# Optimization experiments

Measured on AMD Instinct MI355X. Metric: run time of the kernel, lower is better.

Reference implementation:

```python
import jax, jax.numpy as jnp
import numpy as np

D_MODEL = 256
N_LAYERS = 2
EXPAND = 2
D_INNER = EXPAND * D_MODEL  # 512
D_STATE = 16
D_CONV = 4
DT_RANK = max(1, D_MODEL // 16)  # 16


def _selective_scan(x, dt, B, C, A, D):
    # x, dt: [b, l, d]   B, C: [b, l, n]   A: [d, n]   D: [d]
    dA = jnp.exp(jnp.einsum('bld,dn->bldn', dt, A))          # discretized state matrix
    dBx = jnp.einsum('bld,bln,bld->bldn', dt, B, x)           # dt * B * u

    def step(h, inp):
        dA_t, dBx_t, C_t = inp                                 # [b,d,n],[b,d,n],[b,n]
        h = dA_t * h + dBx_t
        y = jnp.einsum('bdn,bn->bd', h, C_t)
        return h, y

    h0 = jnp.zeros((x.shape[0], A.shape[0], A.shape[1]), x.dtype)
    _, ys = jax.lax.scan(step, h0, (jnp.moveaxis(dA, 1, 0),
                                    jnp.moveaxis(dBx, 1, 0),
                                    jnp.moveaxis(C, 1, 0)))
    return jnp.moveaxis(ys, 0, 1) + x * D                      # [b, l, d]


def _mamba_block(z, in_w, conv_w, conv_b, xp_w, dt_w, dt_b, A_log, Dp, out_w):
    b, l, _ = z.shape
    xz = z @ in_w.T                                            # [b, l, 2*d_inner]
    x, gate = jnp.split(xz, 2, axis=-1)
    # causal depthwise conv1d over time
    xt = jnp.transpose(x, (0, 2, 1))                            # [b, d_inner, l]
    xt = jax.lax.conv_general_dilated(
        xt, conv_w[:, None, :], window_strides=(1,),
        padding=[(D_CONV - 1, 0)], feature_group_count=D_INNER)
    x = jax.nn.silu(jnp.transpose(xt, (0, 2, 1)) + conv_b)      # [b, l, d_inner]
    x_dbl = x @ xp_w.T                                          # [b, l, dt_rank + 2*d_state]
    dt, Bm, Cm = jnp.split(x_dbl, [DT_RANK, DT_RANK + D_STATE], axis=-1)
    dt = jax.nn.softplus(dt @ dt_w.T + dt_b)                    # [b, l, d_inner]
    A = -jnp.exp(A_log)                                         # [d_inner, d_state]
    y = _selective_scan(x, dt, Bm, Cm, A, Dp)
    y = y * jax.nn.silu(gate)
    return y @ out_w.T                                          # [b, l, d_model]


def setup_inputs() -> dict:
    key = jax.random.key(0)
    ks = jax.random.split(key, 9)
    B, L = 2, 4096
    z = jax.random.normal(ks[0], (B, L, D_MODEL), jnp.float32)
    s = 0.02
    in_proj_w = jax.random.normal(ks[1], (N_LAYERS, 2 * D_INNER, D_MODEL), jnp.float32) * s
    conv_w = jax.random.normal(ks[2], (N_LAYERS, D_INNER, D_CONV), jnp.float32) * 0.2
    conv_b = jnp.zeros((N_LAYERS, D_INNER), jnp.float32)
    x_proj_w = jax.random.normal(ks[3], (N_LAYERS, DT_RANK + 2 * D_STATE, D_INNER), jnp.float32) * s
    dt_proj_w = jax.random.normal(ks[4], (N_LAYERS, D_INNER, DT_RANK), jnp.float32) * 0.1
    dt_proj_b = jax.random.uniform(ks[5], (N_LAYERS, D_INNER), jnp.float32, -4.0, -2.0)
    A_log = jnp.log(jnp.broadcast_to(jnp.arange(1, D_STATE + 1, dtype=jnp.float32),
                                     (N_LAYERS, D_INNER, D_STATE)))
    D_param = jnp.ones((N_LAYERS, D_INNER), jnp.float32)
    out_proj_w = jax.random.normal(ks[6], (N_LAYERS, D_MODEL, D_INNER), jnp.float32) * s
    return {"z": z, "in_proj_w": in_proj_w, "conv_w": conv_w, "conv_b": conv_b,
            "x_proj_w": x_proj_w, "dt_proj_w": dt_proj_w, "dt_proj_b": dt_proj_b,
            "A_log": A_log, "D_param": D_param, "out_proj_w": out_proj_w}


def reference(z, in_proj_w, conv_w, conv_b, x_proj_w, dt_proj_w, dt_proj_b,
              A_log, D_param, out_proj_w):
    for i in range(N_LAYERS):
        z = _mamba_block(z, in_proj_w[i], conv_w[i], conv_b[i], x_proj_w[i],
                         dt_proj_w[i], dt_proj_b[i], A_log[i], D_param[i], out_proj_w[i])
    return z
```

## Files before the change

kernel.cpp:

```cpp
#include <hip/hip_runtime.h>
#include <hip/hip_bf16.h>
#include <cstdint>
#include <cstddef>

#define DM   256
#define DI   512
#define DS   16
#define LSEQ 4096
#define BATCH 2
#define BLROWS (BATCH * LSEQ)
#define NCH  128
#define CLEN 32
#define XCP  520

typedef __bf16 bf16x8 __attribute__((ext_vector_type(8)));
typedef float  f32x4  __attribute__((ext_vector_type(4)));
typedef unsigned short u16;
typedef u16 u16x8 __attribute__((ext_vector_type(8)));
typedef u16 u16x4 __attribute__((ext_vector_type(4)));

__device__ __forceinline__ u16 f2bfu(float f) {
    union { float f; unsigned u; } c; c.f = f;
    unsigned u = c.u;
    return (u16)((u + 0x7fffu + ((u >> 16) & 1u)) >> 16);
}
__device__ __forceinline__ float bfu2f(u16 u) {
    union { unsigned u; float f; } c; c.u = ((unsigned)u) << 16; return c.f;
}
__device__ __forceinline__ float siluf(float v) {
    return v * (1.0f / (1.0f + __expf(-v)));
}
__device__ __forceinline__ void gload_lds16(const void* g, void* l) {
    __builtin_amdgcn_global_load_lds(
        (const __attribute__((address_space(1))) unsigned int*)g,
        (__attribute__((address_space(3))) unsigned int*)l, 16, 0, 0);
}

#define N_INW  (2*1024*256)
#define N_OUTW (2*256*512)
#define N_XPW  (2*64*512)
#define N_Z    (BLROWS*DM)
__global__ __launch_bounds__(256) void cast_all_k(
    const float* __restrict__ in_w, const float* __restrict__ out_w,
    const float* __restrict__ xp_w, const float* __restrict__ z,
    u16* __restrict__ inw_bf, u16* __restrict__ outw_bf,
    u16* __restrict__ xpw_bf, u16* __restrict__ z_bf) {
    int i = blockIdx.x * 256 + threadIdx.x;
    if (i < N_INW) {
        inw_bf[i] = f2bfu(in_w[i]);
    } else if (i < N_INW + N_OUTW) {
        int j = i - N_INW;
        outw_bf[j] = f2bfu(out_w[j]);
    } else if (i < N_INW + N_OUTW + N_XPW) {
        int j = i - (N_INW + N_OUTW);
        int k = j & 511, o = (j >> 9) & 63, l = j >> 15;
        xpw_bf[j] = f2bfu((o < 48) ? xp_w[(l * 48 + o) * 512 + k] : 0.0f);
    } else {
        int j = i - (N_INW + N_OUTW + N_XPW);
        z_bf[j] = f2bfu(z[j]);
    }
}

__global__ __launch_bounds__(256) void gemm_in_k(
    const __bf16* __restrict__ A, const __bf16* __restrict__ B,
    u16* __restrict__ Cb, int M, int N, int K) {
    __shared__ __bf16 As[128 * 32];
    __shared__ __bf16 Bs[128 * 32];
    int tid = threadIdx.x, wave = tid >> 6, lane = tid & 63;
    int bm = blockIdx.x * 128, bn = blockIdx.y * 128;
    int wm = (wave & 1) * 64, wn = (wave >> 1) * 64;
    int row = lane & 15, q = lane >> 4;
    int srow = lane >> 2, sseg = lane & 3;
    f32x4 acc[4][4] = {};
    for (int k0 = 0; k0 < K; k0 += 32) {
        #pragma unroll
        for (int i = 0; i < 2; ++i) {
            int r0 = wave * 32 + i * 16;
            gload_lds16(A + (size_t)(bm + r0 + srow) * K + k0 + sseg * 8, As + r0 * 32);
            gload_lds16(B + (size_t)(bn + r0 + srow) * K + k0 + sseg * 8, Bs + r0 * 32);
        }
        __syncthreads();
        bf16x8 af[4], bfr[4];
        #pragma unroll
        for (int mi = 0; mi < 4; ++mi)
            af[mi] = *(const bf16x8*)&As[(wm + mi*16 + row) * 32 + q * 8];
        #pragma unroll
        for (int ni = 0; ni < 4; ++ni)
            bfr[ni] = *(const bf16x8*)&Bs[(wn + ni*16 + row) * 32 + q * 8];
        #pragma unroll
        for (int mi = 0; mi < 4; ++mi)
            #pragma unroll
            for (int ni = 0; ni < 4; ++ni)
                acc[mi][ni] = __builtin_amdgcn_mfma_f32_16x16x32_bf16(
                    af[mi], bfr[ni], acc[mi][ni], 0, 0, 0);
        __syncthreads();
    }
    #pragma unroll
    for (int mi = 0; mi < 4; ++mi)
        #pragma unroll
        for (int r = 0; r < 4; ++r) {
            size_t gr = (size_t)(bm + wm + mi*16 + q*4 + r) * N;
            #pragma unroll
            for (int ni = 0; ni < 4; ++ni)
                Cb[gr + bn + wn + ni*16 + row] = f2bfu(acc[mi][ni][r]);
        }
}

__global__ __launch_bounds__(512) void fused_a_k(
    const u16* __restrict__ xz, const float* __restrict__ cw,
    const float* __restrict__ cb, const __bf16* __restrict__ xpw,
    const float* __restrict__ dtw, const float* __restrict__ dtb,
    const float* __restrict__ Alog,
    u16* __restrict__ xcb, u16* __restrict__ dtob,
    float* __restrict__ BCg, u16* __restrict__ Pb, u16* __restrict__ Sb) {
    __shared__ u16 xc_s[CLEN * XCP];
    __shared__ float xd_s[CLEN * 68];
    int tid = threadIdx.x;
    int c = blockIdx.x, b = blockIdx.y;
    int bl0 = b * LSEQ + c * CLEN;
    int d = tid;

    {
        float w0 = cw[d*4], w1 = cw[d*4+1], w2 = cw[d*4+2], w3 = cw[d*4+3];
        float bias = cb[d];
        float xm3 = 0.f, xm2 = 0.f, xm1 = 0.f;
        int l0 = c * CLEN;
        if (l0 - 3 >= 0) xm3 = bfu2f(xz[(size_t)(bl0 - 3) * 1024 + d]);
        if (l0 - 2 >= 0) xm2 = bfu2f(xz[(size_t)(bl0 - 2) * 1024 + d]);
        if (l0 - 1 >= 0) xm1 = bfu2f(xz[(size_t)(bl0 - 1) * 1024 + d]);
        #pragma unroll 4
        for (int t = 0; t < CLEN; ++t) {
            float xcur = bfu2f(xz[(size_t)(bl0 + t) * 1024 + d]);
            float acc = fmaf(w0, xm3, fmaf(w1, xm2, fmaf(w2, xm1, fmaf(w3, xcur, bias))));
            float v = siluf(acc);
            u16 vb = f2bfu(v);
            xc_s[t * XCP + d] = vb;
            xcb[(size_t)(bl0 + t) * DI + d] = vb;
            xm3 = xm2; xm2 = xm1; xm1 = xcur;
        }
    }
    __syncthreads();

    {
        int wave = tid >> 6, lane = tid & 63;
        int row = lane & 15, q = lane >> 4;
        int mt = wave & 1, nt = wave >> 2;
        nt = wave >> 1;
        f32x4 acc = {0.f, 0.f, 0.f, 0.f};
        #pragma unroll
        for (int kb = 0; kb < 16; ++kb) {
            bf16x8 a = *(const bf16x8*)&xc_s[(mt*16 + row) * XCP + kb*32 + q*8];
            bf16x8 bb = *(const bf16x8*)(xpw + (size_t)(nt*16 + row) * 512 + kb*32 + q*8);
            acc = __builtin_amdgcn_mfma_f32_16x16x32_bf16(a, bb, acc, 0, 0, 0);
        }
        #pragma unroll
        for (int r = 0; r < 4; ++r)
            xd_s[(mt*16 + q*4 + r) * 68 + nt*16 + row] = acc[r];
    }
    __syncthreads();

    for (int i = tid; i < CLEN * 32; i += 512) {
        int t = i >> 5, cc = i & 31;
        BCg[((size_t)(b*NCH + c) * CLEN + t) * 32 + cc] = xd_s[t*68 + 16 + cc];
    }

    {
        float dtwr[16];
        const f32x4* w4 = (const f32x4*)(dtw + (size_t)d * 16);
        #pragma unroll
        for (int g = 0; g < 4; ++g) { f32x4 v = w4[g];
            dtwr[g*4] = v[0]; dtwr[g*4+1] = v[1]; dtwr[g*4+2] = v[2]; dtwr[g*4+3] = v[3]; }
        float dtbv = dtb[d];
        float Ac[16];
        const f32x4* a4 = (const f32x4*)(Alog + (size_t)d * 16);
        #pragma unroll
        for (int g = 0; g < 4; ++g) { f32x4 v = a4[g];
            #pragma unroll
            for (int j = 0; j < 4; ++j) Ac[g*4+j] = -__expf(v[j]); }
        bool fastp = true;
        #pragma unroll
        for (int n = 1; n < 16; ++n)
            fastp = fastp && (fabsf(Ac[n] - (float)(n+1) * Ac[0])
                              <= 1e-4f * fabsf(Ac[n]));
        float p[16], s[16];
        #pragma unroll
        for (int n = 0; n < 16; ++n) { p[n] = 1.0f; s[n] = 0.0f; }
        for (int t = 0; t < CLEN; ++t) {
            float acc = dtbv;
            #pragma unroll
            for (int r = 0; r < 16; ++r) acc = fmaf(xd_s[t*68 + r], dtwr[r], acc);
            float dtv = (acc > 20.0f) ? acc : logf(1.0f + __expf(acc));
            dtob[(size_t)(bl0 + t) * DI + d] = f2bfu(dtv);
            float xv = bfu2f(xc_s[t * XCP + d]);
            float dx = dtv * xv;
            float an[16];
            if (fastp) {
                float a0 = __expf(dtv * Ac[0]);
                an[0] = a0;
                #pragma unroll
                for (int n = 1; n < 16; ++n) an[n] = an[n-1] * a0;
            } else {
                #pragma unroll
                for (int n = 0; n < 16; ++n) an[n] = __expf(dtv * Ac[n]);
            }
            #pragma unroll
            for (int n = 0; n < 16; ++n) {
                s[n] = fmaf(an[n], s[n], xd_s[t*68 + 16 + n] * dx);
                p[n] *= an[n];
            }
        }
        size_t base = ((size_t)(b*NCH + c) * DI + d) * 16;
        u16x8 pv0, pv1, sv0, sv1;
        #pragma unroll
        for (int n = 0; n < 8; ++n) {
            pv0[n] = f2bfu(p[n]);   pv1[n] = f2bfu(p[8+n]);
            sv0[n] = f2bfu(s[n]);   sv1[n] = f2bfu(s[8+n]);
        }
        *(u16x8*)(Pb + base)     = pv0;  *(u16x8*)(Pb + base + 8) = pv1;
        *(u16x8*)(Sb + base)     = sv0;  *(u16x8*)(Sb + base + 8) = sv1;
    }
}

__global__ __launch_bounds__(256) void scanB_k(
    const u16* __restrict__ Pb, const u16* __restrict__ Sb,
    float* __restrict__ H) {
    int i = blockIdx.x * 256 + threadIdx.x;
    int b = i >> 11, j4 = i & 2047;
    f32x4 h = {0.f, 0.f, 0.f, 0.f};
    for (int c = 0; c < NCH; ++c) {
        size_t i4 = (size_t)(b*NCH + c) * 2048 + j4;
        u16x4 pv = ((const u16x4*)Pb)[i4];
        u16x4 sv = ((const u16x4*)Sb)[i4];
        ((f32x4*)H)[i4] = h;
        #pragma unroll
        for (int j = 0; j < 4; ++j) h[j] = fmaf(bfu2f(pv[j]), h[j], bfu2f(sv[j]));
    }
}

__global__ __launch_bounds__(512) void fused_c_k(
    const u16* __restrict__ xcb, const u16* __restrict__ dtob,
    const float* __restrict__ BCg, const float* __restrict__ H,
    const float* __restrict__ Alog, const float* __restrict__ Dp,
    const u16* __restrict__ xz, const __bf16* __restrict__ outw,
    u16* __restrict__ Ob, float* __restrict__ Of) {
    __shared__ u16 y_s[CLEN * XCP];
    __shared__ float BCs[CLEN * 32];
    int tid = threadIdx.x;
    int c = blockIdx.x, b = blockIdx.y;
    int bl0 = b * LSEQ + c * CLEN;
    int d = tid;

    for (int i = tid; i < CLEN * 32; i += 512)
        BCs[i] = BCg[(size_t)(b*NCH + c) * (CLEN*32) + i];

    float Ac[16], h[16];
    {
        const f32x4* a4 = (const f32x4*)(Alog + (size_t)d * 16);
        const f32x4* h4 = (const f32x4*)(H + ((size_t)(b*NCH + c) * DI + d) * 16);
        #pragma unroll
        for (int g = 0; g < 4; ++g) {
            f32x4 av = a4[g]; f32x4 hv = h4[g];
            #pragma unroll
            for (int j = 0; j < 4; ++j) { Ac[g*4+j] = -__expf(av[j]); h[g*4+j] = hv[j]; }
        }
    }
    bool fastp = true;
    #pragma unroll
    for (int n = 1; n < 16; ++n)
        fastp = fastp && (fabsf(Ac[n] - (float)(n+1) * Ac[0]) <= 1e-4f * fabsf(Ac[n]));
    float Dv = Dp[d];
    __syncthreads();

    #pragma unroll 4
    for (int t = 0; t < CLEN; ++t) {
        float dtv = bfu2f(dtob[(size_t)(bl0 + t) * DI + d]);
        float xv  = bfu2f(xcb[(size_t)(bl0 + t) * DI + d]);
        float gv  = bfu2f(xz[(size_t)(bl0 + t) * 1024 + DI + d]);
        float dx = dtv * xv;
        float an[16];
        if (fastp) {
            float a0 = __expf(dtv * Ac[0]);
            an[0] = a0;
            #pragma unroll
            for (int n = 1; n < 16; ++n) an[n] = an[n-1] * a0;
        } else {
            #pragma unroll
            for (int n = 0; n < 16; ++n) an[n] = __expf(dtv * Ac[n]);
        }
        float y = 0.f;
        #pragma unroll
        for (int n = 0; n < 16; ++n) {
            h[n] = fmaf(an[n], h[n], BCs[t*32 + n] * dx);
            y = fmaf(h[n], BCs[t*32 + 16 + n], y);
        }
        float yv = fmaf(xv, Dv, y) * siluf(gv);
        y_s[t * XCP + d] = f2bfu(yv);
    }
    __syncthreads();

    {
        int wave = tid >> 6, lane = tid & 63;
        int row = lane & 15, q = lane >> 4;
        int mt = wave & 1, ng = wave >> 1;
        f32x4 acc[4] = {};
        #pragma unroll
        for (int kb = 0; kb < 16; ++kb) {
            bf16x8 a = *(const bf16x8*)&y_s[(mt*16 + row) * XCP + kb*32 + q*8];
            #pragma unroll
            for (int ni = 0; ni < 4; ++ni) {
                bf16x8 bb = *(const bf16x8*)(outw +
                    (size_t)(ng*64 + ni*16 + row) * 512 + kb*32 + q*8);
                acc[ni] = __builtin_amdgcn_mfma_f32_16x16x32_bf16(a, bb, acc[ni], 0, 0, 0);
            }
        }
        #pragma unroll
        for (int r = 0; r < 4; ++r) {
            size_t gr = (size_t)(bl0 + mt*16 + q*4 + r) * DM;
            #pragma unroll
            for (int ni = 0; ni < 4; ++ni) {
                int gc = ng*64 + ni*16 + row;
                if (Ob) Ob[gr + gc] = f2bfu(acc[ni][r]);
                else    Of[gr + gc] = acc[ni][r];
            }
        }
    }
}

extern "C" void kernel_launch(void* const* d_in, const int* in_sizes, int n_in,
                              void* d_out, int out_size, void* d_ws, size_t ws_size,
                              hipStream_t stream) {
    (void)in_sizes; (void)n_in; (void)out_size; (void)ws_size;
    const float* z_in   = (const float*)d_in[0];
    const float* in_w   = (const float*)d_in[1];
    const float* conv_w = (const float*)d_in[2];
    const float* conv_b = (const float*)d_in[3];
    const float* xp_w   = (const float*)d_in[4];
    const float* dt_w   = (const float*)d_in[5];
    const float* dt_b   = (const float*)d_in[6];
    const float* A_log  = (const float*)d_in[7];
    const float* D_par  = (const float*)d_in[8];
    const float* out_w  = (const float*)d_in[9];
    float* outp = (float*)d_out;

    char* p = (char*)d_ws;
    auto alloc = [&](size_t bytes) { char* r = p; p += (bytes + 255) & ~(size_t)255; return r; };
    u16* z_bf    = (u16*)alloc((size_t)BLROWS*DM*2);
    u16* z2_bf   = (u16*)alloc((size_t)BLROWS*DM*2);
    u16* xz_bf   = (u16*)alloc((size_t)BLROWS*1024*2);
    u16* xc_bf   = (u16*)alloc((size_t)BLROWS*DI*2);
    u16* dt_bf   = (u16*)alloc((size_t)BLROWS*DI*2);
    u16* inw_bf  = (u16*)alloc((size_t)2*1024*256*2);
    u16* outw_bf = (u16*)alloc((size_t)2*256*512*2);
    u16* xpw_bf  = (u16*)alloc((size_t)2*64*512*2);
    float* BCg   = (float*)alloc((size_t)BATCH*NCH*CLEN*32*4);
    u16* Pbuf    = (u16*)alloc((size_t)BATCH*NCH*DI*DS*2);
    u16* Sbuf    = (u16*)alloc((size_t)BATCH*NCH*DI*DS*2);
    float* Hbuf  = (float*)alloc((size_t)BATCH*NCH*DI*DS*4);

    cast_all_k<<<(N_INW + N_OUTW + N_XPW + N_Z)/256, 256, 0, stream>>>(
        in_w, out_w, xp_w, z_in, inw_bf, outw_bf, xpw_bf, z_bf);

    const u16* zcur = z_bf;
    for (int l = 0; l < 2; ++l) {
        gemm_in_k<<<dim3(BLROWS/128, 1024/128), 256, 0, stream>>>(
            (const __bf16*)zcur, (const __bf16*)(inw_bf + (size_t)l*1024*256),
            xz_bf, BLROWS, 1024, 256);
        fused_a_k<<<dim3(NCH, BATCH), 512, 0, stream>>>(
            xz_bf, conv_w + (size_t)l*DI*4, conv_b + (size_t)l*DI,
            (const __bf16*)(xpw_bf + (size_t)l*64*512),
            dt_w + (size_t)l*DI*16, dt_b + (size_t)l*DI,
            A_log + (size_t)l*DI*DS,
            xc_bf, dt_bf, BCg, Pbuf, Sbuf);
        scanB_k<<<16, 256, 0, stream>>>(Pbuf, Sbuf, Hbuf);
        fused_c_k<<<dim3(NCH, BATCH), 512, 0, stream>>>(
            xc_bf, dt_bf, BCg, Hbuf,
            A_log + (size_t)l*DI*DS, D_par + (size_t)l*DI,
            xz_bf, (const __bf16*)(outw_bf + (size_t)l*256*512),
            (l == 0) ? z2_bf : nullptr, (l == 1) ? outp : nullptr);
        zcur = z2_bf;
    }
}
```

Measured before the change: 254.0 us.

## Fuse conv/scan/output stages into one persistent kernel with grid barriers

Merges fused_a_k, scanB_k and fused_c_k into a single kernel of 256 co-resident blocks that synchronise through atomic grid barriers. The inter-chunk state scan becomes a two-level parallel scan across all blocks instead of a 16-block serial loop. Conv output, dt and B/C stay in shared memory, so their global round trips are removed and dt is recomputed in the second pass. In exchange it adds three spin barriers that depend on every block being resident at once, plus redundant softplus work, and the barrier loop breaks out on a timeout.

Measured after the change: 371.7 us. +46.3%, slower.

```diff
diff --git a/kernel.cpp b/kernel.cpp
--- a/kernel.cpp
+++ b/kernel.cpp
@@ -12,6 +12,8 @@
 #define NCH  128
 #define CLEN 32
 #define XCP  520
+#define NBLK 256
+#define NELEM 16384
 
 typedef __bf16 bf16x8 __attribute__((ext_vector_type(8)));
 typedef float  f32x4  __attribute__((ext_vector_type(4)));
@@ -34,6 +36,22 @@
     __builtin_amdgcn_global_load_lds(
         (const __attribute__((address_space(1))) unsigned int*)g,
         (__attribute__((address_space(3))) unsigned int*)l, 16, 0, 0);
+}
+
+__device__ __forceinline__ void gridbar(int* bar) {
+    __syncthreads();
+    if (threadIdx.x == 0) {
+        __threadfence();
+        atomicAdd(bar, 1);
+        int it = 0;
+        while (__hip_atomic_load(bar, __ATOMIC_RELAXED,
+                                 __HIP_MEMORY_SCOPE_AGENT) < NBLK) {
+            __builtin_amdgcn_s_sleep(8);
+            if (++it > (1 << 22)) break;
+        }
+        __threadfence();
+    }
+    __syncthreads();
 }
 
 #define N_INW  (2*1024*256)
@@ -44,7 +62,9 @@
     const float* __restrict__ in_w, const float* __restrict__ out_w,
     const float* __restrict__ xp_w, const float* __restrict__ z,
     u16* __restrict__ inw_bf, u16* __restrict__ outw_bf,
-    u16* __restrict__ xpw_bf, u16* __restrict__ z_bf) {
+    u16* __restrict__ xpw_bf, u16* __restrict__ z_bf,
+    int* __restrict__ bars) {
+    if (blockIdx.x == 0 && threadIdx.x < 16) bars[threadIdx.x] = 0;
     int i = blockIdx.x * 256 + threadIdx.x;
     if (i < N_INW) {
         inw_bf[i] = f2bfu(in_w[i]);
@@ -106,17 +126,22 @@
         }
 }
 
-__global__ __launch_bounds__(512) void fused_a_k(
+__global__ __launch_bounds__(512, 2) void mega_k(
     const u16* __restrict__ xz, const float* __restrict__ cw,
     const float* __restrict__ cb, const __bf16* __restrict__ xpw,
     const float* __restrict__ dtw, const float* __restrict__ dtb,
-    const float* __restrict__ Alog,
-    u16* __restrict__ xcb, u16* __restrict__ dtob,
-    float* __restrict__ BCg, u16* __restrict__ Pb, u16* __restrict__ Sb) {
+    const float* __restrict__ Alog, const float* __restrict__ Dp,
+    const __bf16* __restrict__ outw,
+    u16* __restrict__ Pb, u16* __restrict__ Sb,
+    float* __restrict__ Pagg, float* __restrict__ Sagg,
+    float* __restrict__ Hg,
+    int* __restrict__ bars,
+    u16* __restrict__ Ob, float* __restrict__ Of) {
     __shared__ u16 xc_s[CLEN * XCP];
     __shared__ float xd_s[CLEN * 68];
     int tid = threadIdx.x;
     int c = blockIdx.x, b = blockIdx.y;
+    int flat = b * NCH + c;
     int bl0 = b * LSEQ + c * CLEN;
     int d = tid;
 
@@ -132,10 +157,7 @@
         for (int t = 0; t < CLEN; ++t) {
             float xcur = bfu2f(xz[(size_t)(bl0 + t) * 1024 + d]);
             float acc = fmaf(w0, xm3, fmaf(w1, xm2, fmaf(w2, xm1, fmaf(w3, xcur, bias))));
-            float v = siluf(acc);
-            u16 vb = f2bfu(v);
-            xc_s[t * XCP + d] = vb;
-            xcb[(size_t)(bl0 + t) * DI + d] = vb;
+            xc_s[t * XCP + d] = f2bfu(siluf(acc));
             xm3 = xm2; xm2 = xm1; xm1 = xcur;
         }
     }
@@ -144,8 +166,7 @@
     {
         int wave = tid >> 6, lane = tid & 63;
         int row = lane & 15, q = lane >> 4;
-        int mt = wave & 1, nt = wave >> 2;
-        nt = wave >> 1;
+        int mt = wave & 1, nt = wave >> 1;
         f32x4 acc = {0.f, 0.f, 0.f, 0.f};
         #pragma unroll
         for (int kb = 0; kb < 16; ++kb) {
@@ -158,11 +179,6 @@
             xd_s[(mt*16 + q*4 + r) * 68 + nt*16 + row] = acc[r];
     }
     __syncthreads();
-
-    for (int i = tid; i < CLEN * 32; i += 512) {
-        int t = i >> 5, cc = i & 31;
-        BCg[((size_t)(b*NCH + c) * CLEN + t) * 32 + cc] = xd_s[t*68 + 16 + cc];
-    }
 
     {
         float dtwr[16];
@@ -189,8 +205,8 @@
             float acc = dtbv;
             #pragma unroll
             for (int r = 0; r < 16; ++r) acc = fmaf(xd_s[t*68 + r], dtwr[r], acc);
-            float dtv = (acc > 20.0f) ? acc : logf(1.0f + __expf(acc));
-            dtob[(size_t)(bl0 + t) * DI + d] = f2bfu(dtv);
+            float dtraw = (acc > 20.0f) ? acc : logf(1.0f + __expf(acc));
+            float dtv = bfu2f(f2bfu(dtraw));
             float xv = bfu2f(xc_s[t * XCP + d]);
             float dx = dtv * xv;
             float an[16];
@@ -209,7 +225,7 @@
                 p[n] *= an[n];
             }
         }
-        size_t base = ((size_t)(b*NCH + c) * DI + d) * 16;
+        size_t base = ((size_t)flat * DI + d) * 16;
         u16x8 pv0, pv1, sv0, sv1;
         #pragma unroll
         for (int n = 0; n < 8; ++n) {
@@ -219,82 +235,96 @@
         *(u16x8*)(Pb + base)     = pv0;  *(u16x8*)(Pb + base + 8) = pv1;
         *(u16x8*)(Sb + base)     = sv0;  *(u16x8*)(Sb + base + 8) = sv1;
     }
-}
-
-__global__ __launch_bounds__(256) void scanB_k(
-    const u16* __restrict__ Pb, const u16* __restrict__ Sb,
-    float* __restrict__ H) {
-    int i = blockIdx.x * 256 + threadIdx.x;
-    int b = i >> 11, j4 = i & 2047;
-    f32x4 h = {0.f, 0.f, 0.f, 0.f};
-    for (int c = 0; c < NCH; ++c) {
-        size_t i4 = (size_t)(b*NCH + c) * 2048 + j4;
-        u16x4 pv = ((const u16x4*)Pb)[i4];
-        u16x4 sv = ((const u16x4*)Sb)[i4];
-        ((f32x4*)H)[i4] = h;
-        #pragma unroll
-        for (int j = 0; j < 4; ++j) h[j] = fmaf(bfu2f(pv[j]), h[j], bfu2f(sv[j]));
-    }
-}
-
-__global__ __launch_bounds__(512) void fused_c_k(
-    const u16* __restrict__ xcb, const u16* __restrict__ dtob,
-    const float* __restrict__ BCg, const float* __restrict__ H,
-    const float* __restrict__ Alog, const float* __restrict__ Dp,
-    const u16* __restrict__ xz, const __bf16* __restrict__ outw,
-    u16* __restrict__ Ob, float* __restrict__ Of) {
-    __shared__ u16 y_s[CLEN * XCP];
-    __shared__ float BCs[CLEN * 32];
-    int tid = threadIdx.x;
-    int c = blockIdx.x, b = blockIdx.y;
-    int bl0 = b * LSEQ + c * CLEN;
-    int d = tid;
-
-    for (int i = tid; i < CLEN * 32; i += 512)
-        BCs[i] = BCg[(size_t)(b*NCH + c) * (CLEN*32) + i];
-
-    float Ac[16], h[16];
-    {
+
+    gridbar(&bars[0]);
+
+    int gid = flat * 512 + tid;
+    int sc = gid >> 14, elem = gid & (NELEM - 1);
+    int eb = elem >> 13, elow = elem & 8191;
+    int cbase = eb * NCH + sc * 16;
+    float hl[16], pp[16];
+    {
+        float h = 0.f, p = 1.f;
+        #pragma unroll
+        for (int k = 0; k < 16; ++k) {
+            hl[k] = h; pp[k] = p;
+            size_t a = (size_t)(cbase + k) * 8192 + elow;
+            float Pv = bfu2f(Pb[a]), Sv = bfu2f(Sb[a]);
+            h = fmaf(Pv, h, Sv);
+            p *= Pv;
+        }
+        Pagg[sc * NELEM + elem] = p;
+        Sagg[sc * NELEM + elem] = h;
+    }
+
+    gridbar(&bars[1]);
+
+    {
+        float hsup = 0.f;
+        for (int s2 = 0; s2 < sc; ++s2)
+            hsup = fmaf(Pagg[s2 * NELEM + elem], hsup, Sagg[s2 * NELEM + elem]);
+        #pragma unroll
+        for (int k = 0; k < 16; ++k)
+            Hg[(size_t)(cbase + k) * 8192 + elow] = fmaf(pp[k], hsup, hl[k]);
+    }
+
+    gridbar(&bars[2]);
+
+    {
+        float dtwr[16];
+        const f32x4* w4 = (const f32x4*)(dtw + (size_t)d * 16);
+        #pragma unroll
+        for (int g = 0; g < 4; ++g) { f32x4 v = w4[g];
+            dtwr[g*4] = v[0]; dtwr[g*4+1] = v[1]; dtwr[g*4+2] = v[2]; dtwr[g*4+3] = v[3]; }
+        float dtbv = dtb[d];
+        float Ac[16];
         const f32x4* a4 = (const f32x4*)(Alog + (size_t)d * 16);
-        const f32x4* h4 = (const f32x4*)(H + ((size_t)(b*NCH + c) * DI + d) * 16);
+        #pragma unroll
+        for (int g = 0; g < 4; ++g) { f32x4 v = a4[g];
+            #pragma unroll
+            for (int j = 0; j < 4; ++j) Ac[g*4+j] = -__expf(v[j]); }
+        bool fastp = true;
+        #pragma unroll
+        for (int n = 1; n < 16; ++n)
+            fastp = fastp && (fabsf(Ac[n] - (float)(n+1) * Ac[0])
+                              <= 1e-4f * fabsf(Ac[n]));
+        float h[16];
+        const f32x4* h4 = (const f32x4*)(Hg + ((size_t)flat * DI + d) * 16);
         #pragma unroll
         for (int g = 0; g < 4; ++g) {
-            f32x4 av = a4[g]; f32x4 hv = h4[g];
-            #pragma unroll
-            for (int j = 0; j < 4; ++j) { Ac[g*4+j] = -__expf(av[j]); h[g*4+j] = hv[j]; }
-        }
-    }
-    bool fastp = true;
-    #pragma unroll
-    for (int n = 1; n < 16; ++n)
-        fastp = fastp && (fabsf(Ac[n] - (float)(n+1) * Ac[0]) <= 1e-4f * fabsf(Ac[n]));
-    float Dv = Dp[d];
-    __syncthreads();
-
-    #pragma unroll 4
-    for (int t = 0; t < CLEN; ++t) {
-        float dtv = bfu2f(dtob[(size_t)(bl0 + t) * DI + d]);
-        float xv  = bfu2f(xcb[(size_t)(bl0 + t) * DI + d]);
-        float gv  = bfu2f(xz[(size_t)(bl0 + t) * 1024 + DI + d]);
-        float dx = dtv * xv;
-        float an[16];
-        if (fastp) {
-            float a0 = __expf(dtv * Ac[0]);
-            an[0] = a0;
-            #pragma unroll
-            for (int n = 1; n < 16; ++n) an[n] = an[n-1] * a0;
-        } else {
-            #pragma unroll
-            for (int n = 0; n < 16; ++n) an[n] = __expf(dtv * Ac[n]);
-        }
-        float y = 0.f;
-        #pragma unroll
-        for (int n = 0; n < 16; ++n) {
-            h[n] = fmaf(an[n], h[n], BCs[t*32 + n] * dx);
-            y = fmaf(h[n], BCs[t*32 + 16 + n], y);
-        }
-        float yv = fmaf(xv, Dv, y) * siluf(gv);
-        y_s[t * XCP + d] = f2bfu(yv);
+            f32x4 hv = h4[g];
+            #pragma unroll
+            for (int j = 0; j < 4; ++j) h[g*4+j] = hv[j];
+        }
+        float Dv = Dp[d];
+        for (int t = 0; t < CLEN; ++t) {
+            float acc = dtbv;
+            #pragma unroll
+            for (int r = 0; r < 16; ++r) acc = fmaf(xd_s[t*68 + r], dtwr[r], acc);
+            float dtraw = (acc > 20.0f) ? acc : logf(1.0f + __expf(acc));
+            float dtv = bfu2f(f2bfu(dtraw));
+            float xv  = bfu2f(xc_s[t * XCP + d]);
+            float gv  = bfu2f(xz[(size_t)(bl0 + t) * 1024 + DI + d]);
+            float dx = dtv * xv;
+            float an[16];
+            if (fastp) {
+                float a0 = __expf(dtv * Ac[0]);
+                an[0] = a0;
+                #pragma unroll
+                for (int n = 1; n < 16; ++n) an[n] = an[n-1] * a0;
+            } else {
+                #pragma unroll
+                for (int n = 0; n < 16; ++n) an[n] = __expf(dtv * Ac[n]);
+            }
+            float y = 0.f;
+            #pragma unroll
+            for (int n = 0; n < 16; ++n) {
+                h[n] = fmaf(an[n], h[n], xd_s[t*68 + 16 + n] * dx);
+                y = fmaf(h[n], xd_s[t*68 + 32 + n], y);
+            }
+            float yv = fmaf(xv, Dv, y) * siluf(gv);
+            xc_s[t * XCP + d] = f2bfu(yv);
+        }
     }
     __syncthreads();
 
@@ -305,7 +335,7 @@
         f32x4 acc[4] = {};
         #pragma unroll
         for (int kb = 0; kb < 16; ++kb) {
-            bf16x8 a = *(const bf16x8*)&y_s[(mt*16 + row) * XCP + kb*32 + q*8];
+            bf16x8 a = *(const bf16x8*)&xc_s[(mt*16 + row) * XCP + kb*32 + q*8];
             #pragma unroll
             for (int ni = 0; ni < 4; ++ni) {
                 bf16x8 bb = *(const bf16x8*)(outw +
@@ -347,35 +377,32 @@
     u16* z_bf    = (u16*)alloc((size_t)BLROWS*DM*2);
     u16* z2_bf   = (u16*)alloc((size_t)BLROWS*DM*2);
     u16* xz_bf   = (u16*)alloc((size_t)BLROWS*1024*2);
-    u16* xc_bf   = (u16*)alloc((size_t)BLROWS*DI*2);
-    u16* dt_bf   = (u16*)alloc((size_t)BLROWS*DI*2);
     u16* inw_bf  = (u16*)alloc((size_t)2*1024*256*2);
     u16* outw_bf = (u16*)alloc((size_t)2*256*512*2);
     u16* xpw_bf  = (u16*)alloc((size_t)2*64*512*2);
-    float* BCg   = (float*)alloc((size_t)BATCH*NCH*CLEN*32*4);
     u16* Pbuf    = (u16*)alloc((size_t)BATCH*NCH*DI*DS*2);
     u16* Sbuf    = (u16*)alloc((size_t)BATCH*NCH*DI*DS*2);
     float* Hbuf  = (float*)alloc((size_t)BATCH*NCH*DI*DS*4);
+    float* PaggG = (float*)alloc((size_t)NELEM*8*4);
+    float* SaggG = (float*)alloc((size_t)NELEM*8*4);
+    int* bars    = (int*)alloc(64);
 
     cast_all_k<<<(N_INW + N_OUTW + N_XPW + N_Z)/256, 256, 0, stream>>>(
-        in_w, out_w, xp_w, z_in, inw_bf, outw_bf, xpw_bf, z_bf);
+        in_w, out_w, xp_w, z_in, inw_bf, outw_bf, xpw_bf, z_bf, bars);
 
     const u16* zcur = z_bf;
     for (int l = 0; l < 2; ++l) {
         gemm_in_k<<<dim3(BLROWS/128, 1024/128), 256, 0, stream>>>(
             (const __bf16*)zcur, (const __bf16*)(inw_bf + (size_t)l*1024*256),
             xz_bf, BLROWS, 1024, 256);
-        fused_a_k<<<dim3(NCH, BATCH), 512, 0, stream>>>(
+        mega_k<<<dim3(NCH, BATCH), 512, 0, stream>>>(
             xz_bf, conv_w + (size_t)l*DI*4, conv_b + (size_t)l*DI,
             (const __bf16*)(xpw_bf + (size_t)l*64*512),
             dt_w + (size_t)l*DI*16, dt_b + (size_t)l*DI,
-            A_log + (size_t)l*DI*DS,
-            xc_bf, dt_bf, BCg, Pbuf, Sbuf);
-        scanB_k<<<16, 256, 0, stream>>>(Pbuf, Sbuf, Hbuf);
-        fused_c_k<<<dim3(NCH, BATCH), 512, 0, stream>>>(
-            xc_bf, dt_bf, BCg, Hbuf,
             A_log + (size_t)l*DI*DS, D_par + (size_t)l*DI,
-            xz_bf, (const __bf16*)(outw_bf + (size_t)l*256*512),
+            (const __bf16*)(outw_bf + (size_t)l*256*512),
+            Pbuf, Sbuf, PaggG, SaggG, Hbuf,
+            bars + (size_t)l*4,
             (l == 0) ? z2_bf : nullptr, (l == 1) ? outp : nullptr);
         zcur = z2_bf;
     }
```

## Halve chunk length and replace serial inter-chunk scan with two-level parallel scan

Applied to the files above, without the earlier changes.

Shrinks the scan chunk length from 32 to 16, doubling the number of chunk blocks in the fused pre-scan and post-scan kernels, and reworks their MFMA tiling to a single 16-row tile (split-K with an LDS reduction for x_proj). The old 16-block serial scan over 128 chunks is replaced by a two-pass hierarchical scan that aggregates 16-chunk superchunks and then propagates prefixes, exposing far more threads. It also rounds dt to bf16 before using it in the local scan so the values match those stored for the later kernel, and adds occupancy hints to the launch bounds. The cost is more chunk-state traffic (twice as many P/S/H entries), an extra kernel launch, and redundant prefix work in the second scan pass.

Result: faster. 231.3 us (-8.9%).

```diff
diff --git a/kernel.cpp b/kernel.cpp
--- a/kernel.cpp
+++ b/kernel.cpp
@@ -9,15 +9,15 @@
 #define LSEQ 4096
 #define BATCH 2
 #define BLROWS (BATCH * LSEQ)
-#define NCH  128
-#define CLEN 32
+#define NCH  256
+#define CLEN 16
+#define NSC  16
 #define XCP  520
 
 typedef __bf16 bf16x8 __attribute__((ext_vector_type(8)));
 typedef float  f32x4  __attribute__((ext_vector_type(4)));
 typedef unsigned short u16;
 typedef u16 u16x8 __attribute__((ext_vector_type(8)));
-typedef u16 u16x4 __attribute__((ext_vector_type(4)));
 
 __device__ __forceinline__ u16 f2bfu(float f) {
     union { float f; unsigned u; } c; c.f = f;
@@ -106,7 +106,7 @@
         }
 }
 
-__global__ __launch_bounds__(512) void fused_a_k(
+__global__ __launch_bounds__(512, 4) void fused_a_k(
     const u16* __restrict__ xz, const float* __restrict__ cw,
     const float* __restrict__ cb, const __bf16* __restrict__ xpw,
     const float* __restrict__ dtw, const float* __restrict__ dtb,
@@ -114,9 +114,10 @@
     u16* __restrict__ xcb, u16* __restrict__ dtob,
     float* __restrict__ BCg, u16* __restrict__ Pb, u16* __restrict__ Sb) {
     __shared__ u16 xc_s[CLEN * XCP];
-    __shared__ float xd_s[CLEN * 68];
+    __shared__ float xd_h[2][CLEN * 68];
     int tid = threadIdx.x;
     int c = blockIdx.x, b = blockIdx.y;
+    int flat = b * NCH + c;
     int bl0 = b * LSEQ + c * CLEN;
     int d = tid;
 
@@ -144,24 +145,26 @@
     {
         int wave = tid >> 6, lane = tid & 63;
         int row = lane & 15, q = lane >> 4;
-        int mt = wave & 1, nt = wave >> 2;
-        nt = wave >> 1;
+        int nt = wave & 3, kh = wave >> 2;
         f32x4 acc = {0.f, 0.f, 0.f, 0.f};
         #pragma unroll
-        for (int kb = 0; kb < 16; ++kb) {
-            bf16x8 a = *(const bf16x8*)&xc_s[(mt*16 + row) * XCP + kb*32 + q*8];
-            bf16x8 bb = *(const bf16x8*)(xpw + (size_t)(nt*16 + row) * 512 + kb*32 + q*8);
+        for (int kb = 0; kb < 8; ++kb) {
+            int kk = (kh*8 + kb) * 32;
+            bf16x8 a = *(const bf16x8*)&xc_s[row * XCP + kk + q*8];
+            bf16x8 bb = *(const bf16x8*)(xpw + (size_t)(nt*16 + row) * 512 + kk + q*8);
             acc = __builtin_amdgcn_mfma_f32_16x16x32_bf16(a, bb, acc, 0, 0, 0);
         }
         #pragma unroll
         for (int r = 0; r < 4; ++r)
-            xd_s[(mt*16 + q*4 + r) * 68 + nt*16 + row] = acc[r];
+            xd_h[kh][(q*4 + r) * 68 + nt*16 + row] = acc[r];
     }
     __syncthreads();
-
-    for (int i = tid; i < CLEN * 32; i += 512) {
-        int t = i >> 5, cc = i & 31;
-        BCg[((size_t)(b*NCH + c) * CLEN + t) * 32 + cc] = xd_s[t*68 + 16 + cc];
+    for (int j = tid; j < CLEN * 68; j += 512) xd_h[0][j] += xd_h[1][j];
+    __syncthreads();
+
+    {
+        int t = tid >> 5, cc = tid & 31;
+        BCg[(size_t)flat * (CLEN*32) + tid] = xd_h[0][t*68 + 16 + cc];
     }
 
     {
@@ -188,9 +191,10 @@
         for (int t = 0; t < CLEN; ++t) {
             float acc = dtbv;
             #pragma unroll
-            for (int r = 0; r < 16; ++r) acc = fmaf(xd_s[t*68 + r], dtwr[r], acc);
-            float dtv = (acc > 20.0f) ? acc : logf(1.0f + __expf(acc));
-            dtob[(size_t)(bl0 + t) * DI + d] = f2bfu(dtv);
+            for (int r = 0; r < 16; ++r) acc = fmaf(xd_h[0][t*68 + r], dtwr[r], acc);
+            float dtraw = (acc > 20.0f) ? acc : logf(1.0f + __expf(acc));
+            float dtv = bfu2f(f2bfu(dtraw));
+            dtob[(size_t)(bl0 + t) * DI + d] = f2bfu(dtraw);
             float xv = bfu2f(xc_s[t * XCP + d]);
             float dx = dtv * xv;
             float an[16];
@@ -205,11 +209,11 @@
             }
             #pragma unroll
             for (int n = 0; n < 16; ++n) {
-                s[n] = fmaf(an[n], s[n], xd_s[t*68 + 16 + n] * dx);
+                s[n] = fmaf(an[n], s[n], xd_h[0][t*68 + 16 + n] * dx);
                 p[n] *= an[n];
             }
         }
-        size_t base = ((size_t)(b*NCH + c) * DI + d) * 16;
+        size_t base = ((size_t)flat * DI + d) * 16;
         u16x8 pv0, pv1, sv0, sv1;
         #pragma unroll
         for (int n = 0; n < 8; ++n) {
@@ -221,25 +225,49 @@
     }
 }
 
-__global__ __launch_bounds__(256) void scanB_k(
+__global__ __launch_bounds__(256) void scan1_k(
     const u16* __restrict__ Pb, const u16* __restrict__ Sb,
-    float* __restrict__ H) {
-    int i = blockIdx.x * 256 + threadIdx.x;
-    int b = i >> 11, j4 = i & 2047;
-    f32x4 h = {0.f, 0.f, 0.f, 0.f};
-    for (int c = 0; c < NCH; ++c) {
-        size_t i4 = (size_t)(b*NCH + c) * 2048 + j4;
-        u16x4 pv = ((const u16x4*)Pb)[i4];
-        u16x4 sv = ((const u16x4*)Sb)[i4];
-        ((f32x4*)H)[i4] = h;
-        #pragma unroll
-        for (int j = 0; j < 4; ++j) h[j] = fmaf(bfu2f(pv[j]), h[j], bfu2f(sv[j]));
-    }
-}
-
-__global__ __launch_bounds__(512) void fused_c_k(
+    float* __restrict__ Pagg, float* __restrict__ Sagg) {
+    int gid = blockIdx.x * 256 + threadIdx.x;
+    int scg = gid >> 13, elow = gid & 8191;
+    int b = scg >> 4, sc = scg & 15;
+    int cbase = b * NCH + sc * 16;
+    float h = 0.f, p = 1.f;
+    #pragma unroll
+    for (int k = 0; k < 16; ++k) {
+        size_t a = (size_t)(cbase + k) * 8192 + elow;
+        float Pv = bfu2f(Pb[a]), Sv = bfu2f(Sb[a]);
+        h = fmaf(Pv, h, Sv);
+        p *= Pv;
+    }
+    Pagg[(size_t)scg * 8192 + elow] = p;
+    Sagg[(size_t)scg * 8192 + elow] = h;
+}
+
+__global__ __launch_bounds__(256) void scan2_k(
+    const u16* __restrict__ Pb, const u16* __restrict__ Sb,
+    const float* __restrict__ Pagg, const float* __restrict__ Sagg,
+    float* __restrict__ Hg) {
+    int gid = blockIdx.x * 256 + threadIdx.x;
+    int scg = gid >> 13, elow = gid & 8191;
+    int b = scg >> 4, sc = scg & 15;
+    int cbase = b * NCH + sc * 16;
+    float h = 0.f;
+    for (int s2 = 0; s2 < sc; ++s2) {
+        size_t ai = (size_t)(b*16 + s2) * 8192 + elow;
+        h = fmaf(Pagg[ai], h, Sagg[ai]);
+    }
+    #pragma unroll
+    for (int k = 0; k < 16; ++k) {
+        size_t a = (size_t)(cbase + k) * 8192 + elow;
+        Hg[a] = h;
+        h = fmaf(bfu2f(Pb[a]), h, bfu2f(Sb[a]));
+    }
+}
+
+__global__ __launch_bounds__(512, 4) void fused_c_k(
     const u16* __restrict__ xcb, const u16* __restrict__ dtob,
-    const float* __restrict__ BCg, const float* __restrict__ H,
+    const float* __restrict__ BCg, const float* __restrict__ Hg,
     const float* __restrict__ Alog, const float* __restrict__ Dp,
     const u16* __restrict__ xz, const __bf16* __restrict__ outw,
     u16* __restrict__ Ob, float* __restrict__ Of) {
@@ -247,16 +275,16 @@
     __shared__ float BCs[CLEN * 32];
     int tid = threadIdx.x;
     int c = blockIdx.x, b = blockIdx.y;
+    int flat = b * NCH + c;
     int bl0 = b * LSEQ + c * CLEN;
     int d = tid;
 
-    for (int i = tid; i < CLEN * 32; i += 512)
-        BCs[i] = BCg[(size_t)(b*NCH + c) * (CLEN*32) + i];
+    BCs[tid] = BCg[(size_t)flat * (CLEN*32) + tid];
 
     float Ac[16], h[16];
     {
         const f32x4* a4 = (const f32x4*)(Alog + (size_t)d * 16);
-        const f32x4* h4 = (const f32x4*)(H + ((size_t)(b*NCH + c) * DI + d) * 16);
+        const f32x4* h4 = (const f32x4*)(Hg + ((size_t)flat * DI + d) * 16);
         #pragma unroll
         for (int g = 0; g < 4; ++g) {
             f32x4 av = a4[g]; f32x4 hv = h4[g];
@@ -301,24 +329,23 @@
     {
         int wave = tid >> 6, lane = tid & 63;
         int row = lane & 15, q = lane >> 4;
-        int mt = wave & 1, ng = wave >> 1;
-        f32x4 acc[4] = {};
+        f32x4 acc[2] = {};
         #pragma unroll
         for (int kb = 0; kb < 16; ++kb) {
-            bf16x8 a = *(const bf16x8*)&y_s[(mt*16 + row) * XCP + kb*32 + q*8];
-            #pragma unroll
-            for (int ni = 0; ni < 4; ++ni) {
+            bf16x8 a = *(const bf16x8*)&y_s[row * XCP + kb*32 + q*8];
+            #pragma unroll
+            for (int ni = 0; ni < 2; ++ni) {
                 bf16x8 bb = *(const bf16x8*)(outw +
-                    (size_t)(ng*64 + ni*16 + row) * 512 + kb*32 + q*8);
+                    (size_t)(wave*32 + ni*16 + row) * 512 + kb*32 + q*8);
                 acc[ni] = __builtin_amdgcn_mfma_f32_16x16x32_bf16(a, bb, acc[ni], 0, 0, 0);
             }
         }
         #pragma unroll
         for (int r = 0; r < 4; ++r) {
-            size_t gr = (size_t)(bl0 + mt*16 + q*4 + r) * DM;
-            #pragma unroll
-            for (int ni = 0; ni < 4; ++ni) {
-                int gc = ng*64 + ni*16 + row;
+            size_t gr = (size_t)(bl0 + q*4 + r) * DM;
+            #pragma unroll
+            for (int ni = 0; ni < 2; ++ni) {
+                int gc = wave*32 + ni*16 + row;
                 if (Ob) Ob[gr + gc] = f2bfu(acc[ni][r]);
                 else    Of[gr + gc] = acc[ni][r];
             }
@@ -356,6 +383,8 @@
     u16* Pbuf    = (u16*)alloc((size_t)BATCH*NCH*DI*DS*2);
     u16* Sbuf    = (u16*)alloc((size_t)BATCH*NCH*DI*DS*2);
     float* Hbuf  = (float*)alloc((size_t)BATCH*NCH*DI*DS*4);
+    float* PaggG = (float*)alloc((size_t)BATCH*NSC*8192*4);
+    float* SaggG = (float*)alloc((size_t)BATCH*NSC*8192*4);
 
     cast_all_k<<<(N_INW + N_OUTW + N_XPW + N_Z)/256, 256, 0, stream>>>(
         in_w, out_w, xp_w, z_in, inw_bf, outw_bf, xpw_bf, z_bf);
@@ -371,7 +400,8 @@
             dt_w + (size_t)l*DI*16, dt_b + (size_t)l*DI,
             A_log + (size_t)l*DI*DS,
             xc_bf, dt_bf, BCg, Pbuf, Sbuf);
-        scanB_k<<<16, 256, 0, stream>>>(Pbuf, Sbuf, Hbuf);
+        scan1_k<<<BATCH*NSC*8192/256, 256, 0, stream>>>(Pbuf, Sbuf, PaggG, SaggG);
+        scan2_k<<<BATCH*NSC*8192/256, 256, 0, stream>>>(Pbuf, Sbuf, PaggG, SaggG, Hbuf);
         fused_c_k<<<dim3(NCH, BATCH), 512, 0, stream>>>(
             xc_bf, dt_bf, BCg, Hbuf,
             A_log + (size_t)l*DI*DS, D_par + (size_t)l*DI,
```
